# Performance work log

Hardware: AMD Instinct MI355X
Metric: run time of the kernel (lower is better)

## Reference

```python
import jax, jax.numpy as jnp
import numpy as np

N_NODES = 50000
N_EDGES = 800000
DIM = 128
LN_EPS = 1e-5


def setup_inputs() -> dict:
    key = jax.random.key(0)
    k1, k2, k3, k4 = jax.random.split(key, 4)
    h = jax.random.normal(k1, (N_NODES, DIM), dtype=jnp.float32)
    edge_index = jax.random.randint(k2, (2, N_EDGES), 0, N_NODES, dtype=jnp.int64)
    W = jax.random.normal(k3, (DIM, DIM), dtype=jnp.float32) / np.sqrt(DIM)
    b = jnp.zeros((DIM,), dtype=jnp.float32)
    gamma = jnp.ones((DIM,), dtype=jnp.float32)
    beta = jnp.zeros((DIM,), dtype=jnp.float32)
    t = jnp.zeros((), dtype=jnp.float32)
    return {"t": t, "h": h, "edge_index": edge_index, "batch_size": N_NODES,
            "W": W, "b": b, "gamma": gamma, "beta": beta}


def _gcn_conv(h, edge_index, W, b):
    """PyG-style GCNConv: D^{-1/2} (A+I) D^{-1/2} (h W) + b."""
    N = h.shape[0]
    loops = jnp.arange(N, dtype=edge_index.dtype)
    src = jnp.concatenate([edge_index[0], loops])  # [E+N]
    dst = jnp.concatenate([edge_index[1], loops])  # [E+N]
    # degree (with self loops) on destination nodes
    deg = jax.ops.segment_sum(jnp.ones_like(dst, dtype=h.dtype), dst, num_segments=N)
    dinv = jnp.where(deg > 0, jax.lax.rsqrt(deg), 0.0)
    norm = dinv[src] * dinv[dst]                    # [E+N]
    xw = h @ W                                      # [N, D]
    msg = xw[src] * norm[:, None]                   # gather + scale, [E+N, D]
    agg = jax.ops.segment_sum(msg, dst, num_segments=N)  # scatter-add, [N, D]
    return agg + b


def reference(t, h, edge_index, batch_size, W, b, gamma, beta):
    if h.ndim == 1:
        h = h[None, :]
    dh = _gcn_conv(h, edge_index, W, b)
    # LayerNorm over feature dim, then tanh
    mean = jnp.mean(dh, axis=-1, keepdims=True)
    var = jnp.mean(jnp.square(dh - mean), axis=-1, keepdims=True)
    dh = (dh - mean) * jax.lax.rsqrt(var + LN_EPS) * gamma + beta
    dh = jnp.tanh(dh)
    return (dh, jnp.zeros_like(edge_index), jnp.zeros_like(jnp.asarray(batch_size)))
```

## Files before the change

kernel.cpp:

```cpp
#include <hip/hip_runtime.h>
#include <math.h>

#define NN 50000
#define NE 800000
#define D  128
#define SCAN_CHUNK 1024
#define NSCAN ((NN + SCAN_CHUNK - 1) / SCAN_CHUNK)

typedef __attribute__((ext_vector_type(8))) short bf16x8;
typedef __attribute__((ext_vector_type(4))) float f32x4;

__device__ __forceinline__ unsigned short f32_to_bf16(float f) {
    unsigned u = __float_as_uint(f);
    u = u + 0x7FFFu + ((u >> 16) & 1u);
    return (unsigned short)(u >> 16);
}

__global__ __launch_bounds__(256) void k_pre(const float* __restrict__ h,
                                             unsigned* __restrict__ hb,
                                             const float* __restrict__ Wg,
                                             unsigned short* __restrict__ Wb,
                                             const int* __restrict__ ei,
                                             int* __restrict__ deg,
                                             unsigned short* __restrict__ rank,
                                             int* __restrict__ outtail, int tailN) {
    int t = blockIdx.x * 256 + threadIdx.x;
    float2 v = ((const float2*)h)[t];
    unsigned a = __float_as_uint(v.x);
    unsigned b = __float_as_uint(v.y);
    a = a + 0x7FFFu + ((a >> 16) & 1u);
    b = b + 0x7FFFu + ((b >> 16) & 1u);
    hb[t] = (a >> 16) | (b & 0xFFFF0000u);
    if (t < NE) {
        int dst = ei[NE + t];
        rank[t] = (unsigned short)atomicAdd(&deg[dst], 1);
    }
    if (t < D * D) {
        int k = t >> 7, n = t & 127;
        int frag = (n >> 4) * 256 + (k >> 5) * 64 + ((k >> 3) & 3) * 16 + (n & 15);
        Wb[frag * 8 + (k & 7)] = f32_to_bf16(Wg[t]);
    }
    if (t < tailN) outtail[t] = 0;
}

__global__ __launch_bounds__(256) void k_gemmz(const unsigned* __restrict__ hb,
                                               const unsigned short* __restrict__ Wb,
                                               unsigned short* __restrict__ zb) {
    int tid = threadIdx.x;
    int w = tid >> 6, lane = tid & 63;
    int quad = lane >> 4, lo = lane & 15;
    int rowBase = blockIdx.x * 64 + w * 16;
    int rowA = rowBase + lo; if (rowA > NN - 1) rowA = NN - 1;
    const uint4* hb4 = (const uint4*)hb;
    const uint4* Wb4 = (const uint4*)Wb;

    bf16x8 af[4];
#pragma unroll
    for (int kt = 0; kt < 4; kt++) {
        uint4 ta = hb4[(size_t)rowA * 16 + kt * 4 + quad];
        af[kt] = __builtin_bit_cast(bf16x8, ta);
    }

    f32x4 acc[8];
#pragma unroll
    for (int nt = 0; nt < 8; nt++) acc[nt] = (f32x4){0.f, 0.f, 0.f, 0.f};

#pragma unroll
    for (int kt = 0; kt < 4; kt++) {
#pragma unroll
        for (int nt = 0; nt < 8; nt++) {
            uint4 tb = Wb4[nt * 256 + kt * 64 + lane];
            bf16x8 bfv = __builtin_bit_cast(bf16x8, tb);
            acc[nt] = __builtin_amdgcn_mfma_f32_16x16x32_bf16(af[kt], bfv, acc[nt], 0, 0, 0);
        }
    }

#pragma unroll
    for (int reg = 0; reg < 4; reg++) {
        int row = rowBase + quad * 4 + reg;
        if (row < NN) {
#pragma unroll
            for (int nt = 0; nt < 8; nt++)
                zb[(size_t)row * D + nt * 16 + lo] = f32_to_bf16(acc[nt][reg]);
        }
    }
}

__global__ __launch_bounds__(256) void k_scan(const int* __restrict__ deg,
                                              int* __restrict__ partial,
                                              int* __restrict__ flag,
                                              int* __restrict__ rowoff,
                                              float* __restrict__ dinv) {
    __shared__ int sbuf[256];
    int t = threadIdx.x;
    int bid = blockIdx.x;
    int base = bid * SCAN_CHUNK + t * 4;
    int d[4]; int s = 0;
#pragma unroll
    for (int j = 0; j < 4; j++) {
        int i = base + j;
        d[j] = 0;
        if (i < NN) {
            d[j] = deg[i];
            s += d[j];
            dinv[i] = rsqrtf((float)d[j] + 1.0f);
        }
    }
    sbuf[t] = s; __syncthreads();
    for (int off = 1; off < 256; off <<= 1) {
        int v = (t >= off) ? sbuf[t - off] : 0;
        __syncthreads();
        sbuf[t] += v;
        __syncthreads();
    }
    if (t == 0) {
        atomicExch(&partial[bid], sbuf[255]);
        __threadfence();
        atomicAdd(flag, 1);
        while (atomicAdd(flag, 0) < NSCAN) {}
    }
    __syncthreads();

    int lane = t & 63;
    int pv = (lane < NSCAN && lane < bid) ? atomicAdd(&partial[lane], 0) : 0;
#pragma unroll
    for (int off = 32; off > 0; off >>= 1) pv += __shfl_xor(pv, off, 64);

    int ex = sbuf[t] - s + pv;
#pragma unroll
    for (int j = 0; j < 4; j++) {
        int i = base + j;
        if (i < NN) {
            rowoff[i] = ex;
            ex += d[j];
            if (i == NN - 1) rowoff[NN] = ex;
        }
    }
}

__global__ __launch_bounds__(320) void k_fill(const int* __restrict__ ei,
                                              const int* __restrict__ rowoff,
                                              const unsigned short* __restrict__ rank,
                                              int* __restrict__ csr) {
    int t = blockIdx.x * 320 + threadIdx.x;
    int4 s4 = ((const int4*)ei)[t];
    int4 d4 = ((const int4*)(ei + NE))[t];
    ushort4 r4 = ((const ushort4*)rank)[t];
    csr[rowoff[d4.x] + r4.x] = s4.x;
    csr[rowoff[d4.y] + r4.y] = s4.y;
    csr[rowoff[d4.z] + r4.z] = s4.z;
    csr[rowoff[d4.w] + r4.w] = s4.w;
}

__global__ __launch_bounds__(256) void k_gather_ln(
        const int* __restrict__ rowoff, const int* __restrict__ csr,
        const float* __restrict__ dinv, const unsigned* __restrict__ zbu,
        const float* __restrict__ bias, const float* __restrict__ gamma,
        const float* __restrict__ beta, float* __restrict__ out) {
    int tid = threadIdx.x;
    int w = tid >> 6, lane = tid & 63;
    int rowBase = blockIdx.x * 16 + w * 4;

    float2 x[4];
    for (int r = 0; r < 4; r++) {
        int row = rowBase + r;
        float dn = dinv[row];
        unsigned zr = zbu[(size_t)row * 64 + lane];
        float2 a;
        a.x = dn * __uint_as_float(zr << 16);
        a.y = dn * __uint_as_float(zr & 0xFFFF0000u);
        int start = rowoff[row], end = rowoff[row + 1];
        for (int c = start; c < end; c += 64) {
            int m = end - c; if (m > 64) m = 64;
            int s = 0; float wv = 0.f;
            if (lane < m) { s = csr[c + lane]; wv = dinv[s]; }
            int j = 0;
            for (; j + 7 < m; j += 8) {
                unsigned p[8]; float wj[8];
#pragma unroll
                for (int q = 0; q < 8; q++) {
                    int sq = __shfl(s, j + q, 64);
                    wj[q]  = __shfl(wv, j + q, 64);
                    p[q]   = zbu[(size_t)sq * 64 + lane];
                }
#pragma unroll
                for (int q = 0; q < 8; q++) {
                    a.x = fmaf(wj[q], __uint_as_float(p[q] << 16), a.x);
                    a.y = fmaf(wj[q], __uint_as_float(p[q] & 0xFFFF0000u), a.y);
                }
            }
            for (; j < m; j++) {
                int   sj = __shfl(s,  j, 64);
                float fj = __shfl(wv, j, 64);
                unsigned pj = zbu[(size_t)sj * 64 + lane];
                a.x = fmaf(fj, __uint_as_float(pj << 16), a.x);
                a.y = fmaf(fj, __uint_as_float(pj & 0xFFFF0000u), a.y);
            }
        }
        a.x *= dn; a.y *= dn;
        x[r] = a;
    }

    float2 bi = ((const float2*)bias)[lane];
    float2 ga = ((const float2*)gamma)[lane];
    float2 be = ((const float2*)beta)[lane];
#pragma unroll
    for (int r = 0; r < 4; r++) {
        int row = rowBase + r;
        float y0 = x[r].x + bi.x;
        float y1 = x[r].y + bi.y;
        float s = y0 + y1;
#pragma unroll
        for (int off = 32; off > 0; off >>= 1) s += __shfl_xor(s, off, 64);
        float m = s * (1.0f / 128.0f);
        float v0 = y0 - m, v1 = y1 - m;
        float vs = v0 * v0 + v1 * v1;
#pragma unroll
        for (int off = 32; off > 0; off >>= 1) vs += __shfl_xor(vs, off, 64);
        float rstd = rsqrtf(vs * (1.0f / 128.0f) + 1e-5f);
        float2 o;
        o.x = tanhf(v0 * rstd * ga.x + be.x);
        o.y = tanhf(v1 * rstd * ga.y + be.y);
        *(float2*)&out[(size_t)row * D + lane * 2] = o;
    }
}

extern "C" void kernel_launch(void* const* d_in, const int* in_sizes, int n_in,
                              void* d_out, int out_size, void* d_ws, size_t ws_size,
                              hipStream_t stream) {
    const float* h     = (const float*)d_in[1];
    const int*   ei    = (const int*)  d_in[2];
    const float* Wg    = (const float*)d_in[4];
    const float* b     = (const float*)d_in[5];
    const float* gamma = (const float*)d_in[6];
    const float* beta  = (const float*)d_in[7];
    float* out = (float*)d_out;

    int*            deg    = (int*)d_ws;
    int*            flag   = deg + NN;
    int*            partial= flag + 1;
    unsigned short* rank   = (unsigned short*)(partial + 64);
    int*            rowoff = (int*)(rank + NE);
    float*          dinv   = (float*)(rowoff + NN + 1);
    int*            csr    = (int*)(dinv + NN);
    unsigned*       hb     = (unsigned*)(csr + NE);
    unsigned short* Wb     = (unsigned short*)(hb + (size_t)NN * 64);

    int tailN = out_size - NN * D;
    int* outtail = (int*)(out + (size_t)NN * D);

    hipMemsetAsync(deg, 0, (NN + 1) * sizeof(int), stream);
    k_pre      <<<12500, 256, 0, stream>>>(h, hb, Wg, Wb, ei, deg, rank, outtail, tailN);
    k_gemmz    <<<782,   256, 0, stream>>>(hb, Wb, (unsigned short*)hb);
    k_scan     <<<NSCAN, 256, 0, stream>>>(deg, partial, flag, rowoff, dinv);
    k_fill     <<<625,   320, 0, stream>>>(ei, rowoff, rank, csr);
    k_gather_ln<<<NN / 16, 256, 0, stream>>>(rowoff, csr, dinv, hb, b, gamma, beta, out);
}
```

Measured before the change: 209.6 us.

## Fuse preprocessing into GEMM kernel and convert h to bf16 on the fly

Merges the preprocessing kernel (bf16 conversion of h, W fragment packing, degree atomics, tail zeroing) into the GEMM kernel. W is converted into LDS per block, and h is read as fp32 and converted in registers, so the bf16 copy of h is never written or re-read. Degree counting now processes four edges per thread with vectorized loads. In exchange, every block repacks the full W matrix from global memory and uses 32KB of LDS, which may lower occupancy.

```diff
diff --git a/kernel.cpp b/kernel.cpp
--- a/kernel.cpp
+++ b/kernel.cpp
@@ -6,6 +6,7 @@
 #define D  128
 #define SCAN_CHUNK 1024
 #define NSCAN ((NN + SCAN_CHUNK - 1) / SCAN_CHUNK)
+#define PG_BLOCKS 782
 
 typedef __attribute__((ext_vector_type(8))) short bf16x8;
 typedef __attribute__((ext_vector_type(4))) float f32x4;
@@ -16,60 +17,65 @@
     return (unsigned short)(u >> 16);
 }
 
-__global__ __launch_bounds__(256) void k_pre(const float* __restrict__ h,
-                                             unsigned* __restrict__ hb,
-                                             const float* __restrict__ Wg,
-                                             unsigned short* __restrict__ Wb,
-                                             const int* __restrict__ ei,
-                                             int* __restrict__ deg,
-                                             unsigned short* __restrict__ rank,
-                                             int* __restrict__ outtail, int tailN) {
-    int t = blockIdx.x * 256 + threadIdx.x;
-    float2 v = ((const float2*)h)[t];
-    unsigned a = __float_as_uint(v.x);
-    unsigned b = __float_as_uint(v.y);
-    a = a + 0x7FFFu + ((a >> 16) & 1u);
-    b = b + 0x7FFFu + ((b >> 16) & 1u);
-    hb[t] = (a >> 16) | (b & 0xFFFF0000u);
-    if (t < NE) {
-        int dst = ei[NE + t];
-        rank[t] = (unsigned short)atomicAdd(&deg[dst], 1);
-    }
-    if (t < D * D) {
-        int k = t >> 7, n = t & 127;
+__global__ __launch_bounds__(256) void k_prep_gemm(
+        const float* __restrict__ h,  const float* __restrict__ Wg,
+        const int* __restrict__ ei,   int* __restrict__ deg,
+        unsigned short* __restrict__ rank,
+        unsigned short* __restrict__ zb,
+        int* __restrict__ outtail, int tailN) {
+    __shared__ unsigned short Wl[D * D];
+    int tid = threadIdx.x;
+
+#pragma unroll 4
+    for (int i = 0; i < 64; i++) {
+        int e = i * 256 + tid;
+        int k = e >> 7, n = e & 127;
         int frag = (n >> 4) * 256 + (k >> 5) * 64 + ((k >> 3) & 3) * 16 + (n & 15);
-        Wb[frag * 8 + (k & 7)] = f32_to_bf16(Wg[t]);
-    }
-    if (t < tailN) outtail[t] = 0;
-}
-
-__global__ __launch_bounds__(256) void k_gemmz(const unsigned* __restrict__ hb,
-                                               const unsigned short* __restrict__ Wb,
-                                               unsigned short* __restrict__ zb) {
-    int tid = threadIdx.x;
+        Wl[frag * 8 + (k & 7)] = f32_to_bf16(Wg[e]);
+    }
+
+    int g = blockIdx.x * 256 + tid;
+    if (g < NE / 4) {
+        int4 d4 = ((const int4*)(ei + NE))[g];
+        ushort4 r;
+        r.x = (unsigned short)atomicAdd(&deg[d4.x], 1);
+        r.y = (unsigned short)atomicAdd(&deg[d4.y], 1);
+        r.z = (unsigned short)atomicAdd(&deg[d4.z], 1);
+        r.w = (unsigned short)atomicAdd(&deg[d4.w], 1);
+        ((ushort4*)rank)[g] = r;
+    }
+    for (int i = g; i < tailN; i += PG_BLOCKS * 256) outtail[i] = 0;
+
     int w = tid >> 6, lane = tid & 63;
     int quad = lane >> 4, lo = lane & 15;
     int rowBase = blockIdx.x * 64 + w * 16;
     int rowA = rowBase + lo; if (rowA > NN - 1) rowA = NN - 1;
-    const uint4* hb4 = (const uint4*)hb;
-    const uint4* Wb4 = (const uint4*)Wb;
+    const float4* h4 = (const float4*)h;
 
     bf16x8 af[4];
 #pragma unroll
     for (int kt = 0; kt < 4; kt++) {
-        uint4 ta = hb4[(size_t)rowA * 16 + kt * 4 + quad];
-        af[kt] = __builtin_bit_cast(bf16x8, ta);
-    }
+        float4 u = h4[(size_t)rowA * 32 + kt * 8 + quad * 2];
+        float4 v = h4[(size_t)rowA * 32 + kt * 8 + quad * 2 + 1];
+        bf16x8 a;
+        a[0] = (short)f32_to_bf16(u.x); a[1] = (short)f32_to_bf16(u.y);
+        a[2] = (short)f32_to_bf16(u.z); a[3] = (short)f32_to_bf16(u.w);
+        a[4] = (short)f32_to_bf16(v.x); a[5] = (short)f32_to_bf16(v.y);
+        a[6] = (short)f32_to_bf16(v.z); a[7] = (short)f32_to_bf16(v.w);
+        af[kt] = a;
+    }
+    __syncthreads();
 
     f32x4 acc[8];
 #pragma unroll
     for (int nt = 0; nt < 8; nt++) acc[nt] = (f32x4){0.f, 0.f, 0.f, 0.f};
 
+    const uint4* Wl4 = (const uint4*)Wl;
 #pragma unroll
     for (int kt = 0; kt < 4; kt++) {
 #pragma unroll
         for (int nt = 0; nt < 8; nt++) {
-            uint4 tb = Wb4[nt * 256 + kt * 64 + lane];
+            uint4 tb = Wl4[nt * 256 + kt * 64 + lane];
             bf16x8 bfv = __builtin_bit_cast(bf16x8, tb);
             acc[nt] = __builtin_amdgcn_mfma_f32_16x16x32_bf16(af[kt], bfv, acc[nt], 0, 0, 0);
         }
@@ -243,16 +249,14 @@
     int*            rowoff = (int*)(rank + NE);
     float*          dinv   = (float*)(rowoff + NN + 1);
     int*            csr    = (int*)(dinv + NN);
-    unsigned*       hb     = (unsigned*)(csr + NE);
-    unsigned short* Wb     = (unsigned short*)(hb + (size_t)NN * 64);
+    unsigned short* zb     = (unsigned short*)(csr + NE);
 
     int tailN = out_size - NN * D;
     int* outtail = (int*)(out + (size_t)NN * D);
 
     hipMemsetAsync(deg, 0, (NN + 1) * sizeof(int), stream);
-    k_pre      <<<12500, 256, 0, stream>>>(h, hb, Wg, Wb, ei, deg, rank, outtail, tailN);
-    k_gemmz    <<<782,   256, 0, stream>>>(hb, Wb, (unsigned short*)hb);
-    k_scan     <<<NSCAN, 256, 0, stream>>>(deg, partial, flag, rowoff, dinv);
-    k_fill     <<<625,   320, 0, stream>>>(ei, rowoff, rank, csr);
-    k_gather_ln<<<NN / 16, 256, 0, stream>>>(rowoff, csr, dinv, hb, b, gamma, beta, out);
-}
+    k_prep_gemm<<<PG_BLOCKS, 256, 0, stream>>>(h, Wg, ei, deg, rank, zb, outtail, tailN);
+    k_scan     <<<NSCAN,     256, 0, stream>>>(deg, partial, flag, rowoff, dinv);
+    k_fill     <<<625,       320, 0, stream>>>(ei, rowoff, rank, csr);
+    k_gather_ln<<<NN / 16,   256, 0, stream>>>(rowoff, csr, dinv, (const unsigned*)zb, b, gamma, beta, out);
+}
```

After: 203.6 us. 2.9% less time.
